# Kernel tuning notes

Hardware: AMD Instinct MI355X
Metric: run time of the kernel (lower is better)

Reference implementation:

```python
import jax, jax.numpy as jnp
import numpy as np

H_IMG, W_IMG = 256, 256
FX = FY = 300.0
CX, CY = W_IMG / 2.0, H_IMG / 2.0
NEAR, FAR = 0.01, 100.0
MAX_RADIUS = 64.0
N_GAUSS = 4096


def quat_to_rot(q):
    q = q / jnp.linalg.norm(q, axis=-1, keepdims=True)
    w, x, y, z = q[..., 0], q[..., 1], q[..., 2], q[..., 3]
    R = jnp.stack([
        1 - 2 * y * y - 2 * z * z, 2 * x * y - 2 * w * z, 2 * x * z + 2 * w * y,
        2 * x * y + 2 * w * z, 1 - 2 * x * x - 2 * z * z, 2 * y * z - 2 * w * x,
        2 * x * z - 2 * w * y, 2 * y * z + 2 * w * x, 1 - 2 * x * x - 2 * y * y,
    ], axis=-1)
    return R.reshape(q.shape[:-1] + (3, 3))


def setup_inputs():
    key = jax.random.key(0)
    k1, k2, k3, k4, k5, k6 = jax.random.split(key, 6)
    xy = jax.random.normal(k1, (N_GAUSS, 2), jnp.float32) * 2.0
    z = -(jax.random.uniform(k2, (N_GAUSS, 1), jnp.float32) * 6.0 + 2.0)  # depths in [2, 8]
    positions = jnp.concatenate([xy, z], axis=1)
    scales = jax.random.uniform(k3, (N_GAUSS, 3), jnp.float32) * 0.10 + 0.02
    rotations = jax.random.normal(k4, (N_GAUSS, 4), jnp.float32)
    colors = jax.random.uniform(k5, (N_GAUSS, 3), jnp.float32)
    opacities = jax.random.uniform(k6, (N_GAUSS,), jnp.float32) * 0.8 + 0.1
    view_matrix = jnp.eye(4, dtype=jnp.float32)
    return {"positions": positions, "scales": scales, "rotations": rotations,
            "colors": colors, "opacities": opacities, "view_matrix": view_matrix}


def _render(positions, scales, rotations, colors, opacities, view_matrix):
    N = positions.shape[0]
    pts = jnp.concatenate([positions, jnp.ones((N, 1), positions.dtype)], axis=1)
    pc = (view_matrix @ pts.T).T[:, :3]  # camera-space points (N,3)
    x, y, z = pc[:, 0], pc[:, 1], pc[:, 2]
    depths = -z
    z_safe = jnp.clip(jnp.abs(z), 0.01) * jnp.sign(z + 1e-8)
    z2 = z_safe * z_safe
    # 3D covariance = (Rcam R S)(Rcam R S)^T
    R = quat_to_rot(rotations)
    R_cam = view_matrix[:3, :3] @ R
    RS = R_cam * scales[:, None, :]  # right-multiply by diag(scales)
    cov3d = RS @ jnp.swapaxes(RS, -1, -2)
    # perspective Jacobian (N,2,3)
    zr = jnp.zeros_like(x)
    J = jnp.stack([
        jnp.stack([FX / -z_safe, zr, FX * x / z2], axis=-1),
        jnp.stack([zr, FY / z_safe, FY * y / z2], axis=-1),
    ], axis=-2)
    cov2d = J @ cov3d @ jnp.swapaxes(J, -1, -2)
    u = FX * x / -z_safe + CX
    v = FY * -y / -z_safe + CY
    # effective radius: 3 sigma from max eigenvalue of 2x2 covariance
    a, b = cov2d[:, 0, 0], cov2d[:, 0, 1]
    c, d = cov2d[:, 1, 0], cov2d[:, 1, 1]
    tr = a + d
    det = jnp.clip(a * d - b * c, 1e-6)
    disc = jnp.clip(tr * tr - 4.0 * det, 0.0)
    lam = (tr + jnp.sqrt(disc)) * 0.5
    radii = jnp.minimum(3.0 * jnp.sqrt(jnp.clip(lam, 1e-6)), MAX_RADIUS)
    # depth sort (front to back)
    order = jnp.argsort(depths)
    u, v, a, b, c, d = u[order], v[order], a[order], b[order], c[order], d[order]
    radii, depths = radii[order], depths[order]
    colors_s, op_s = colors[order], opacities[order]
    # visibility culling: zero opacity instead of compaction (same math, static shapes)
    visible = (depths > NEAR) & (depths < FAR)
    visible &= (u + radii > 0) & (u - radii < W_IMG)
    visible &= (v + radii > 0) & (v - radii < H_IMG)
    op_s = jnp.where(visible, op_s, 0.0)
    # regularized 2x2 inverse (pinv of PD matrix == inverse)
    ar, dr = a + 1e-4, d + 1e-4
    inv_det = 1.0 / (ar * dr - b * c)
    ia, ib, ic, idd = dr * inv_det, -b * inv_det, -c * inv_det, ar * inv_det
    px = jnp.arange(W_IMG, dtype=jnp.float32)[None, :]
    py = jnp.arange(H_IMG, dtype=jnp.float32)[:, None]

    def step(carry, g):
        acc_c, acc_a = carry
        mx, my, gia, gib, gic, gid, r, col, o = g
        dx = px - mx  # (1,W)
        dy = py - my  # (H,1)
        power = -0.5 * (gia * dx * dx + (gib + gic) * dx * dy + gid * dy * dy)
        # bounding-box mask replicating the torch tile bounds [int(m-r), int(m+r)+1)
        inside = ((px >= jnp.trunc(mx - r)) & (px <= jnp.trunc(mx + r))
                  & (py >= jnp.trunc(my - r)) & (py <= jnp.trunc(my + r)))
        alpha = jnp.where(inside, o * jnp.exp(power), 0.0)
        w = alpha * (1.0 - acc_a)  # front-to-back over-compositing
        return (acc_c + w[..., None] * col, acc_a + w), None

    acc0 = (jnp.zeros((H_IMG, W_IMG, 3), jnp.float32),
            jnp.zeros((H_IMG, W_IMG), jnp.float32))
    (acc_c, acc_a), _ = jax.lax.scan(
        step, acc0, (u, v, ia, ib, ic, idd, radii, colors_s, op_s))
    bg = jnp.zeros(3, jnp.float32)
    img = acc_c + (1.0 - acc_a)[..., None] * bg
    return jnp.transpose(img, (2, 0, 1))  # (3,H,W)


def reference(positions, scales, rotations, colors, opacities, view_matrix):
    return _render(positions, scales, rotations, colors, opacities, view_matrix)
```

## Files before the change

### kernel.cpp

```cpp
#include <hip/hip_runtime.h>
#include <hip/hip_fp16.h>
#include <math.h>

#define N_G   4096
#define CAP   1024
#define W_IMG 256
#define H_IMG 256

__global__ __launch_bounds__(64) void prep(
    const float* __restrict__ pos, const float* __restrict__ scl,
    const float* __restrict__ rot, const float* __restrict__ col,
    const float* __restrict__ opa, const float* __restrict__ vm,
    float4* __restrict__ gaussU, short4* __restrict__ bbhU,
    float* __restrict__ depthU)
{
  const int i = blockIdx.x * 64 + threadIdx.x;
  if (i >= N_G) return;
  const float FX=300.f, FY=300.f, CXc=128.f, CYc=128.f;
  const float HLOG2E = 0.72134752f;
  float V00=vm[0],V01=vm[1],V02=vm[2],V03=vm[3];
  float V10=vm[4],V11=vm[5],V12=vm[6],V13=vm[7];
  float V20=vm[8],V21=vm[9],V22=vm[10],V23=vm[11];
  float p0=pos[3*i], p1=pos[3*i+1], p2=pos[3*i+2];
  float X = V00*p0+V01*p1+V02*p2+V03;
  float Y = V10*p0+V11*p1+V12*p2+V13;
  float Z = V20*p0+V21*p1+V22*p2+V23;
  float depth = -Z;
  float zp = Z + 1e-8f;
  float sgn = (zp>0.f)?1.f:((zp<0.f)?-1.f:0.f);
  float z_safe = fmaxf(fabsf(Z), 0.01f) * sgn;
  float z2 = z_safe*z_safe;
  float qw=rot[4*i], qx=rot[4*i+1], qy=rot[4*i+2], qz=rot[4*i+3];
  float qi = 1.f/sqrtf(qw*qw+qx*qx+qy*qy+qz*qz);
  qw*=qi; qx*=qi; qy*=qi; qz*=qi;
  float R00=1.f-2.f*qy*qy-2.f*qz*qz, R01=2.f*qx*qy-2.f*qw*qz, R02=2.f*qx*qz+2.f*qw*qy;
  float R10=2.f*qx*qy+2.f*qw*qz, R11=1.f-2.f*qx*qx-2.f*qz*qz, R12=2.f*qy*qz-2.f*qw*qx;
  float R20=2.f*qx*qz-2.f*qw*qy, R21=2.f*qy*qz+2.f*qw*qx, R22=1.f-2.f*qx*qx-2.f*qy*qy;
  float C00=V00*R00+V01*R10+V02*R20, C01=V00*R01+V01*R11+V02*R21, C02=V00*R02+V01*R12+V02*R22;
  float C10=V10*R00+V11*R10+V12*R20, C11=V10*R01+V11*R11+V12*R21, C12=V10*R02+V11*R12+V12*R22;
  float C20=V20*R00+V21*R10+V22*R20, C21=V20*R01+V21*R11+V22*R21, C22=V20*R02+V21*R12+V22*R22;
  float s0=scl[3*i], s1=scl[3*i+1], s2=scl[3*i+2];
  float S00=C00*s0,S01=C01*s1,S02=C02*s2;
  float S10=C10*s0,S11=C11*s1,S12=C12*s2;
  float S20=C20*s0,S21=C21*s1,S22=C22*s2;
  float c00=S00*S00+S01*S01+S02*S02;
  float c01=S00*S10+S01*S11+S02*S12;
  float c02=S00*S20+S01*S21+S02*S22;
  float c11=S10*S10+S11*S11+S12*S12;
  float c12=S10*S20+S11*S21+S12*S22;
  float c22=S20*S20+S21*S21+S22*S22;
  float j00=FX/(-z_safe), j02=FX*X/z2;
  float j11=FY/z_safe,    j12=FY*Y/z2;
  float M00=j00*c00+j02*c02, M01=j00*c01+j02*c12, M02=j00*c02+j02*c22;
  float M10=j11*c01+j12*c02, M11=j11*c11+j12*c12, M12=j11*c12+j12*c22;
  float a =M00*j00+M02*j02;
  float b =M01*j11+M02*j12;
  float c_=M10*j00+M12*j02;
  float d =M11*j11+M12*j12;
  float u = FX*X/(-z_safe)+CXc;
  float v = FY*(-Y)/(-z_safe)+CYc;
  float tr=a+d;
  float det=fmaxf(a*d-b*c_, 1e-6f);
  float disc=fmaxf(tr*tr-4.f*det, 0.f);
  float lam=(tr+sqrtf(disc))*0.5f;
  float radius=fminf(3.f*sqrtf(fmaxf(lam,1e-6f)), 64.f);
  bool vis = (depth>0.01f)&&(depth<100.f)
          && (u+radius>0.f)&&(u-radius<(float)W_IMG)
          && (v+radius>0.f)&&(v-radius<(float)H_IMG);
  float o = vis ? opa[i] : 0.f;
  float ar=a+1e-4f, dr=d+1e-4f;
  float inv=1.f/(ar*dr-b*c_);
  short4 bb = make_short4(1000, -1000, 1000, -1000);
  if (o>0.f) {
    bb.x=(short)truncf(u-radius); bb.y=(short)truncf(u+radius);
    bb.z=(short)truncf(v-radius); bb.w=(short)truncf(v+radius);
  }
  unsigned hrg = (unsigned)__half_as_ushort(__float2half_rn(col[3*i]))
               | ((unsigned)__half_as_ushort(__float2half_rn(col[3*i+1]))<<16);
  depthU[i] = depth;
  bbhU[i]   = bb;
  gaussU[2*i]   = make_float4(u, v, (dr*inv)*HLOG2E,
                              ((-b*inv)+(-c_*inv))*HLOG2E);
  gaussU[2*i+1] = make_float4((ar*inv)*HLOG2E, log2f(o),
                              __uint_as_float(hrg), col[3*i+2]);
}

__global__ __launch_bounds__(1024) void render(
    const short4* __restrict__ bbhU, const float4* __restrict__ gaussU,
    const float* __restrict__ depthU, float* __restrict__ out)
{
  __shared__ __align__(16) unsigned long long keys[CAP];
  __shared__ float4 gp[CAP*2];
  __shared__ short4 bbh[CAP];
  __shared__ float4 res[16][64];
  __shared__ int lcnt;

  const int tid = threadIdx.x, wv = tid>>6, lane = tid&63;
  const int bid = (int)((blockIdx.x * 331u) & 511u);
  const int RX0=(bid&15)*16, RY0=(bid>>4)*8;
  const int RX1=RX0+15, RY1=RY0+7;

  if (tid==0) lcnt=0;
  __syncthreads();

  {
    short4 bb[4];
    #pragma unroll
    for (int c4=0;c4<4;c4++) bb[c4]=bbhU[(wv*4+c4)*64+lane];
    #pragma unroll
    for (int c4=0;c4<4;c4++) {
      int idx=(wv*4+c4)*64+lane;
      bool pred=(bb[c4].y>=RX0)&&(bb[c4].x<=RX1)&&(bb[c4].w>=RY0)&&(bb[c4].z<=RY1);
      unsigned long long m=__ballot(pred);
      if (m) {
        int bse=0;
        if (lane==0) bse=atomicAdd(&lcnt, __popcll(m));
        bse=__shfl(bse,0);
        if (pred) {
          int p=bse+__popcll(m&((1ull<<lane)-1ull));
          if (p<CAP)
            keys[p]=((unsigned long long)__float_as_uint(depthU[idx])<<12)
                   |(unsigned)idx;
        }
      }
    }
  }
  __syncthreads();
  const int len = (lcnt<CAP)?lcnt:CAP;

  if (tid<len) {
    unsigned long long kj=keys[tid];
    int idx=(int)(kj&4095u);
    float4 g0=gaussU[2*idx];
    float4 g1=gaussU[2*idx+1];
    short4 b0=bbhU[idx];
    int r=0;
    const ulonglong2* k2=(const ulonglong2*)keys;
    int n2=len>>1;
    for(int s2=0;s2<n2;s2++){
      ulonglong2 kv=k2[s2];
      r += (kv.x<kj)+(kv.y<kj);
    }
    if(len&1) r += (keys[len-1]<kj);
    gp[2*r]  =g0;
    gp[2*r+1]=g1;
    bbh[r]   =b0;
  }
  __syncthreads();

  const int t=wv>>3, seg=wv&7;
  const int TX0=RX0+t*8, TY0=RY0, TX1=TX0+7, TY1=TY0+7;
  const int ipx=TX0+(lane&7), ipy=TY0+(lane>>3);
  const float px=(float)ipx, py=(float)ipy;
  const int segLen=(len+7)>>3;
  const int s=seg*segLen;
  int e=s+segLen; if(e>len) e=len;
  float aR=0.f,aG=0.f,aB=0.f,aA=0.f;
  for(int k0=s;k0<e;k0+=64){
    int kk=k0+lane;
    bool ok=false;
    if(kk<e){
      short4 bb=bbh[kk];
      ok=(bb.y>=TX0)&&(bb.x<=TX1)&&(bb.w>=TY0)&&(bb.z<=TY1);
    }
    unsigned long long mm=__ballot(ok);
    if(mm){
      int k=k0+__builtin_ctzll(mm); mm&=mm-1;
      short4 bb=bbh[k];
      float4 A=gp[2*k], B=gp[2*k+1];
      while(mm){
        int kn=k0+__builtin_ctzll(mm); mm&=mm-1;
        short4 bbn=bbh[kn];
        float4 An=gp[2*kn], Bn=gp[2*kn+1];
        float dx=px-A.x, dy=py-A.y;
        float q2=A.z*dx*dx + A.w*dx*dy + B.x*dy*dy;
        bool inside=(ipx>=bb.x)&&(ipx<=bb.y)&&(ipy>=bb.z)&&(ipy<=bb.w);
        float ex=__builtin_amdgcn_exp2f(B.y-q2);
        float alpha= inside ? ex : 0.f;
        float w=alpha*(1.f-aA);
        unsigned hrg=__float_as_uint(B.z);
        float cR=__half2float(__ushort_as_half((unsigned short)(hrg&0xFFFFu)));
        float cG=__half2float(__ushort_as_half((unsigned short)(hrg>>16)));
        aR+=w*cR; aG+=w*cG; aB+=w*B.w; aA+=w;
        bb=bbn; A=An; B=Bn;
      }
      float dx=px-A.x, dy=py-A.y;
      float q2=A.z*dx*dx + A.w*dx*dy + B.x*dy*dy;
      bool inside=(ipx>=bb.x)&&(ipx<=bb.y)&&(ipy>=bb.z)&&(ipy<=bb.w);
      float ex=__builtin_amdgcn_exp2f(B.y-q2);
      float alpha= inside ? ex : 0.f;
      float w=alpha*(1.f-aA);
      unsigned hrg=__float_as_uint(B.z);
      float cR=__half2float(__ushort_as_half((unsigned short)(hrg&0xFFFFu)));
      float cG=__half2float(__ushort_as_half((unsigned short)(hrg>>16)));
      aR+=w*cR; aG+=w*cG; aB+=w*B.w; aA+=w;
    }
    if(__ballot(aA<=0.9999f)==0ull) break;
  }
  res[wv][lane]=make_float4(aR,aG,aB,aA);
  __syncthreads();

  if(seg==0){
    float4 P=res[wv][lane];
    #pragma unroll
    for(int w=1;w<8;w++){
      float4 Q=res[wv+w][lane];
      float tr_=1.f-P.w;
      P.x+=tr_*Q.x; P.y+=tr_*Q.y; P.z+=tr_*Q.z; P.w+=tr_*Q.w;
    }
    out[0*H_IMG*W_IMG + ipy*W_IMG + ipx]=P.x;
    out[1*H_IMG*W_IMG + ipy*W_IMG + ipx]=P.y;
    out[2*H_IMG*W_IMG + ipy*W_IMG + ipx]=P.z;
  }
}

extern "C" void kernel_launch(void* const* d_in, const int* in_sizes, int n_in,
                              void* d_out, int out_size, void* d_ws, size_t ws_size,
                              hipStream_t stream)
{
  const float* pos=(const float*)d_in[0];
  const float* scl=(const float*)d_in[1];
  const float* rot=(const float*)d_in[2];
  const float* col=(const float*)d_in[3];
  const float* opa=(const float*)d_in[4];
  const float* vm =(const float*)d_in[5];
  float* out=(float*)d_out;
  char* ws=(char*)d_ws;
  float4* gaussU=(float4*)(ws);
  short4* bbhU  =(short4*)(ws + 128*1024);
  float*  depthU=(float*) (ws + 160*1024);
  prep<<<N_G/64, 64, 0, stream>>>(pos,scl,rot,col,opa,vm,gaussU,bbhU,depthU);
  render<<<512, 1024, 0, stream>>>(bbhU,gaussU,depthU,out);
}
```

Baseline: 19.01 us.

## Pack 8-pixel tile bounds with depth and split rank-sort across two thread halves

Prep now writes a packed int2 per Gaussian holding its bounding box in 8-pixel tile units as signed bytes, plus its raw depth bits. The render cull reads this single 8-byte record instead of the separate bbox and depth arrays, and tests overlap in tile coordinates. When a region has at most 512 candidates, the counting rank sort is split so two thread halves each scan half the keys and sum their partial ranks through shared memory. This shortens the serial comparison loop at the cost of an extra barrier. Culling at 8-pixel tile granularity matches the old pixel-exact test only because region bounds align to multiples of 8.

```diff
diff --git a/kernel.cpp b/kernel.cpp
--- a/kernel.cpp
+++ b/kernel.cpp
@@ -12,7 +12,7 @@
     const float* __restrict__ rot, const float* __restrict__ col,
     const float* __restrict__ opa, const float* __restrict__ vm,
     float4* __restrict__ gaussU, short4* __restrict__ bbhU,
-    float* __restrict__ depthU)
+    int2* __restrict__ pkU)
 {
   const int i = blockIdx.x * 64 + threadIdx.x;
   if (i >= N_G) return;
@@ -71,14 +71,18 @@
   float ar=a+1e-4f, dr=d+1e-4f;
   float inv=1.f/(ar*dr-b*c_);
   short4 bb = make_short4(1000, -1000, 1000, -1000);
+  int btp = (127 & 0xFF) | ((-128 & 0xFF)<<8) | ((127 & 0xFF)<<16) | (-128<<24);
   if (o>0.f) {
     bb.x=(short)truncf(u-radius); bb.y=(short)truncf(u+radius);
     bb.z=(short)truncf(v-radius); bb.w=(short)truncf(v+radius);
+    int tx0=((int)bb.x)>>3, tx1=((int)bb.y)>>3;
+    int ty0=((int)bb.z)>>3, ty1=((int)bb.w)>>3;
+    btp = (tx0 & 0xFF) | ((tx1 & 0xFF)<<8) | ((ty0 & 0xFF)<<16) | (ty1<<24);
   }
   unsigned hrg = (unsigned)__half_as_ushort(__float2half_rn(col[3*i]))
                | ((unsigned)__half_as_ushort(__float2half_rn(col[3*i+1]))<<16);
-  depthU[i] = depth;
   bbhU[i]   = bb;
+  pkU[i]    = make_int2(btp, (int)__float_as_uint(depth));
   gaussU[2*i]   = make_float4(u, v, (dr*inv)*HLOG2E,
                               ((-b*inv)+(-c_*inv))*HLOG2E);
   gaussU[2*i+1] = make_float4((ar*inv)*HLOG2E, log2f(o),
@@ -86,31 +90,37 @@
 }
 
 __global__ __launch_bounds__(1024) void render(
-    const short4* __restrict__ bbhU, const float4* __restrict__ gaussU,
-    const float* __restrict__ depthU, float* __restrict__ out)
+    const int2* __restrict__ pkU, const short4* __restrict__ bbhU,
+    const float4* __restrict__ gaussU, float* __restrict__ out)
 {
   __shared__ __align__(16) unsigned long long keys[CAP];
   __shared__ float4 gp[CAP*2];
   __shared__ short4 bbh[CAP];
   __shared__ float4 res[16][64];
   __shared__ int lcnt;
+  int* pr = (int*)res;
 
   const int tid = threadIdx.x, wv = tid>>6, lane = tid&63;
   const int bid = (int)((blockIdx.x * 331u) & 511u);
   const int RX0=(bid&15)*16, RY0=(bid>>4)*8;
-  const int RX1=RX0+15, RY1=RY0+7;
+  const int rtx0=RX0>>3, rtx1=(RX0+15)>>3, rty=RY0>>3;
 
   if (tid==0) lcnt=0;
   __syncthreads();
 
   {
-    short4 bb[4];
+    int2 pk[4];
     #pragma unroll
-    for (int c4=0;c4<4;c4++) bb[c4]=bbhU[(wv*4+c4)*64+lane];
+    for (int c4=0;c4<4;c4++) pk[c4]=pkU[(wv*4+c4)*64+lane];
     #pragma unroll
     for (int c4=0;c4<4;c4++) {
       int idx=(wv*4+c4)*64+lane;
-      bool pred=(bb[c4].y>=RX0)&&(bb[c4].x<=RX1)&&(bb[c4].w>=RY0)&&(bb[c4].z<=RY1);
+      int w=pk[c4].x;
+      int bx=(int)(signed char)(w);
+      int by=(int)(signed char)(w>>8);
+      int bz=(int)(signed char)(w>>16);
+      int bw_=(w>>24);
+      bool pred=(by>=rtx0)&&(bx<=rtx1)&&(bw_>=rty)&&(bz<=rty);
       unsigned long long m=__ballot(pred);
       if (m) {
         int bse=0;
@@ -119,7 +129,7 @@
         if (pred) {
           int p=bse+__popcll(m&((1ull<<lane)-1ull));
           if (p<CAP)
-            keys[p]=((unsigned long long)__float_as_uint(depthU[idx])<<12)
+            keys[p]=((unsigned long long)(unsigned)pk[c4].y<<12)
                    |(unsigned)idx;
         }
       }
@@ -127,24 +137,52 @@
   }
   __syncthreads();
   const int len = (lcnt<CAP)?lcnt:CAP;
-
-  if (tid<len) {
-    unsigned long long kj=keys[tid];
-    int idx=(int)(kj&4095u);
-    float4 g0=gaussU[2*idx];
-    float4 g1=gaussU[2*idx+1];
-    short4 b0=bbhU[idx];
-    int r=0;
+  const bool split = (len<=512);
+
+  if (split) {
     const ulonglong2* k2=(const ulonglong2*)keys;
-    int n2=len>>1;
-    for(int s2=0;s2<n2;s2++){
-      ulonglong2 kv=k2[s2];
-      r += (kv.x<kj)+(kv.y<kj);
-    }
-    if(len&1) r += (keys[len-1]<kj);
-    gp[2*r]  =g0;
-    gp[2*r+1]=g1;
-    bbh[r]   =b0;
+    const int n2=len>>1, nA=n2>>1;
+    float4 g0, g1; short4 b0;
+    if (tid<len) {
+      unsigned long long kj=keys[tid];
+      int idx=(int)(kj&4095u);
+      g0=gaussU[2*idx];
+      g1=gaussU[2*idx+1];
+      b0=bbhU[idx];
+      int r=0;
+      for(int s2=0;s2<nA;s2++){ ulonglong2 kv=k2[s2]; r+=(kv.x<kj)+(kv.y<kj); }
+      pr[tid]=r;
+    } else if (tid>=512 && tid-512<len) {
+      int j=tid-512;
+      unsigned long long kj=keys[j];
+      int r=0;
+      for(int s2=nA;s2<n2;s2++){ ulonglong2 kv=k2[s2]; r+=(kv.x<kj)+(kv.y<kj); }
+      if(len&1) r += (keys[len-1]<kj);
+      pr[tid]=r;
+    }
+    __syncthreads();
+    if (tid<len) {
+      int r=pr[tid]+pr[512+tid];
+      gp[2*r]  =g0;
+      gp[2*r+1]=g1;
+      bbh[r]   =b0;
+    }
+  } else {
+    if (tid<len) {
+      unsigned long long kj=keys[tid];
+      int idx=(int)(kj&4095u);
+      float4 g0=gaussU[2*idx];
+      float4 g1=gaussU[2*idx+1];
+      short4 b0=bbhU[idx];
+      int r=0;
+      const ulonglong2* k2=(const ulonglong2*)keys;
+      int n2=len>>1;
+      for(int s2=0;s2<n2;s2++){ ulonglong2 kv=k2[s2]; r+=(kv.x<kj)+(kv.y<kj); }
+      if(len&1) r += (keys[len-1]<kj);
+      gp[2*r]  =g0;
+      gp[2*r+1]=g1;
+      bbh[r]   =b0;
+    }
   }
   __syncthreads();
 
@@ -228,7 +266,7 @@
   char* ws=(char*)d_ws;
   float4* gaussU=(float4*)(ws);
   short4* bbhU  =(short4*)(ws + 128*1024);
-  float*  depthU=(float*) (ws + 160*1024);
-  prep<<<N_G/64, 64, 0, stream>>>(pos,scl,rot,col,opa,vm,gaussU,bbhU,depthU);
-  render<<<512, 1024, 0, stream>>>(bbhU,gaussU,depthU,out);
+  int2*   pkU   =(int2*)  (ws + 160*1024);
+  prep<<<N_G/64, 64, 0, stream>>>(pos,scl,rot,col,opa,vm,gaussU,bbhU,pkU);
+  render<<<512, 1024, 0, stream>>>(pkU,bbhU,gaussU,out);
 }
```

New measurement: 18.59 us. 2.2% less time.
